# Kernel tuning notes

Measured on AMD Instinct MI355X. Metric: run time of the kernel, lower is better.

## Reference

```python
import jax, jax.numpy as jnp
import numpy as np

jax.config.update('jax_enable_x64', True)

RES = 0.1
HASH_SIZE = 2 ** 20
D = 120
HEADS = 8
HEAD_DIM = D // HEADS  # 15
MOD_T = 201
BMIN = np.array([-2.6, -8.1, 0.0], dtype=np.float32)
BMAX = np.array([4.6, 4.7, 3.1], dtype=np.float32)
PRIMES = np.array([73856093, 19349669, 83492791], dtype=np.int64)
M = 200000


def _build_buffer():
    axes = [np.arange(BMIN[i], BMAX[i], RES, dtype=np.float32) for i in range(3)]
    g = np.meshgrid(*axes, indexing='ij')
    coords = np.stack(g, axis=-1).reshape(-1, 3)
    n = coords.shape[0]
    grid = np.floor(coords / RES).astype(np.int64)
    h = np.remainder((grid * PRIMES).sum(-1), HASH_SIZE)
    buf = np.full(HASH_SIZE, n, dtype=np.int64)
    # loop assigns in increasing i and keeps the first => min index per hash slot
    np.minimum.at(buf, h, np.arange(n, dtype=np.int64))
    buf = np.where(buf == n, -1, buf)
    return buf, n


def setup_inputs() -> dict:
    key = jax.random.key(0)
    ks = jax.random.split(key, 9)
    buf, n_vox = _build_buffer()
    pts = jnp.asarray(BMIN) + jax.random.uniform(ks[0], (M, 3), dtype=jnp.float32) * jnp.asarray(BMAX - BMIN)
    times = jax.random.randint(ks[1], (M,), 0, 1000, dtype=jnp.int64)
    scale = float(1.0 / np.sqrt(D))
    return {
        'query_pts': pts,
        'query_times': times,
        'buffer_voxel_index': jnp.asarray(buf),
        'static_features': 0.01 * jax.random.normal(ks[2], (n_vox, D), dtype=jnp.float32),
        'dynamic_features': 0.01 * jax.random.normal(ks[3], (n_vox, D), dtype=jnp.float32),
        'time_embeddings': 0.01 * jax.random.normal(ks[4], (MOD_T, D), dtype=jnp.float32),
        'fusion_td_w': scale * jax.random.normal(ks[5], (4, D, D), dtype=jnp.float32),
        'fusion_td_b': jnp.zeros((4, D), dtype=jnp.float32),
        'fusion_sd_w': scale * jax.random.normal(ks[6], (4, D, D), dtype=jnp.float32),
        'fusion_sd_b': jnp.zeros((4, D), dtype=jnp.float32),
    }


def _fusion(a, b, W, B):
    # LocalSelfAttentionFusion: 2-token multi-head self-attention over [a; b],
    # returning the attended first token. W/B stack (q, k, v, out) projections.
    m = a.shape[0]
    tok = jnp.stack([a, b], axis=1)  # [M, 2, D]
    q = (tok @ W[0] + B[0]).reshape(m, 2, HEADS, HEAD_DIM)
    k = (tok @ W[1] + B[1]).reshape(m, 2, HEADS, HEAD_DIM)
    v = (tok @ W[2] + B[2]).reshape(m, 2, HEADS, HEAD_DIM)
    s = jnp.einsum('mqhd,mkhd->mhqk', q, k) * np.float32(1.0 / np.sqrt(HEAD_DIM))
    p = jax.nn.softmax(s, axis=-1)  # [M, H, 2, 2]
    o = jnp.einsum('mhqk,mkhd->mqhd', p, v).reshape(m, 2, D)
    return (o @ W[3] + B[3])[:, 0]  # fused token, [M, D]


def reference(query_pts, query_times, buffer_voxel_index, static_features, dynamic_features,
              time_embeddings, fusion_td_w, fusion_td_b, fusion_sd_w, fusion_sd_b):
    grid = jnp.floor(query_pts / RES).astype(jnp.int64)
    h = jnp.remainder((grid * jnp.asarray(PRIMES)).sum(-1), HASH_SIZE)
    v_idx = buffer_voxel_index[h]              # [M]
    valid = v_idx >= 0
    vi = jnp.where(valid, v_idx, 0)            # safe gather index
    ti = jnp.remainder(query_times, MOD_T)
    sf = static_features[vi]                   # [M, D]
    df = dynamic_features[vi]                  # [M, D]
    te = time_embeddings[ti]                   # [M, D]
    cond = _fusion(df, te, fusion_td_w, fusion_td_b)
    fused = _fusion(sf, cond, fusion_sd_w, fusion_sd_b)
    return jnp.where(valid[:, None], fused, jnp.float32(0))
```

## Files before the change

### kernel.cpp

```cpp
#include <hip/hip_runtime.h>
#include <math.h>

#define DD   120
#define KPAD 128
#define KP   136
#define MT   64
#define NTHR 512
#define HASH_MASK 1048575LL
#define MODT 201

typedef short  short8  __attribute__((ext_vector_type(8)));
typedef float  floatx4 __attribute__((ext_vector_type(4)));

__device__ __forceinline__ unsigned short f2b(float f) {
    __bf16 h = (__bf16)f;
    return __builtin_bit_cast(unsigned short, h);
}
__device__ __forceinline__ float b2f(unsigned short u) {
    unsigned int x = ((unsigned int)u) << 16;
    return __builtin_bit_cast(float, x);
}

__global__ __launch_bounds__(256)
void prep_weights(const float* __restrict__ td_w, const float* __restrict__ sd_w,
                  unsigned short* __restrict__ wt)
{
    int idx = blockIdx.x * 256 + threadIdx.x;
    int mat = idx >> 14;
    int n   = (idx >> 7) & 127;
    int k   = idx & 127;
    const float* src = (mat < 4) ? (td_w + mat * DD * DD) : (sd_w + (mat - 4) * DD * DD);
    float v = (n < DD && k < DD) ? src[k * DD + n] : 0.f;
    wt[idx] = f2b(v);
}

__global__ __launch_bounds__(128)
void prep_te(const float* __restrict__ temb, const float* __restrict__ td_w,
             const float* __restrict__ td_b,
             unsigned short* __restrict__ k1t, unsigned short* __restrict__ v1t)
{
    int t = blockIdx.x;
    int n = threadIdx.x;
    float a1 = 0.f, a2 = 0.f;
    if (n < DD) {
        a1 = td_b[DD + n];
        a2 = td_b[2 * DD + n];
        const float* te = temb + t * DD;
        const float* w1 = td_w + 1 * DD * DD;
        const float* w2 = td_w + 2 * DD * DD;
        for (int k = 0; k < DD; k++) {
            float x = te[k];
            a1 = fmaf(x, w1[k * DD + n], a1);
            a2 = fmaf(x, w2[k * DD + n], a2);
        }
    }
    k1t[t * KPAD + n] = f2b(a1);
    v1t[t * KPAD + n] = f2b(a2);
}

__device__ __forceinline__ void gemm_tile(const unsigned short* IN,
                                          const unsigned short* __restrict__ WT,
                                          const float* __restrict__ bias,
                                          unsigned short* OUT,
                                          int lm, int lq, int n0)
{
    const int n = n0 + lm;
    short8 bfr[4];
#pragma unroll
    for (int ks = 0; ks < 4; ks++)
        bfr[ks] = *(const short8*)(WT + n * KPAD + ks * 32 + lq * 8);
    float bv = (n < DD) ? bias[n] : 0.f;
#pragma unroll
    for (int mt = 0; mt < 4; mt++) {
        floatx4 acc = {0.f, 0.f, 0.f, 0.f};
#pragma unroll
        for (int ks = 0; ks < 4; ks++) {
            short8 a = *(const short8*)(IN + (mt * 16 + lm) * KP + ks * 32 + lq * 8);
            acc = __builtin_amdgcn_mfma_f32_16x16x32_bf16(a, bfr[ks], acc, 0, 0, 0);
        }
#pragma unroll
        for (int r = 0; r < 4; r++)
            OUT[(mt * 16 + lq * 4 + r) * KP + n] = f2b(acc[r] + bv);
    }
}

__device__ __forceinline__ void gemm_out(const unsigned short* IN,
                                         const unsigned short* __restrict__ WT,
                                         const float* __restrict__ bias,
                                         float* __restrict__ out,
                                         const int* s_valid, int pbase, int Mpts,
                                         int lm, int lq, int n0)
{
    const int n = n0 + lm;
    short8 bfr[4];
#pragma unroll
    for (int ks = 0; ks < 4; ks++)
        bfr[ks] = *(const short8*)(WT + n * KPAD + ks * 32 + lq * 8);
    float bv = (n < DD) ? bias[n] : 0.f;
#pragma unroll
    for (int mt = 0; mt < 4; mt++) {
        floatx4 acc = {0.f, 0.f, 0.f, 0.f};
#pragma unroll
        for (int ks = 0; ks < 4; ks++) {
            short8 a = *(const short8*)(IN + (mt * 16 + lm) * KP + ks * 32 + lq * 8);
            acc = __builtin_amdgcn_mfma_f32_16x16x32_bf16(a, bfr[ks], acc, 0, 0, 0);
        }
        if (n < DD) {
#pragma unroll
            for (int r = 0; r < 4; r++) {
                int row = mt * 16 + lq * 4 + r;
                int gp = pbase + row;
                if (gp < Mpts)
                    out[(size_t)gp * DD + n] = s_valid[row] ? (acc[r] + bv) : 0.f;
            }
        }
    }
}

__device__ __forceinline__ void attn(const unsigned short* Q, const unsigned short* K0,
                                     const unsigned short* K1, const unsigned short* V0,
                                     const unsigned short* V1, unsigned short* DEST,
                                     int tid)
{
    int p = tid >> 3, h = tid & 7;
    int base = p * KP + h * 15;
    float s0 = 0.f, s1 = 0.f;
#pragma unroll
    for (int j = 0; j < 15; j++) {
        float q = b2f(Q[base + j]);
        s0 = fmaf(q, b2f(K0[base + j]), s0);
        s1 = fmaf(q, b2f(K1[base + j]), s1);
    }
    const float scale = 0.2581988897471611f;
    s0 *= scale; s1 *= scale;
    float mx = fmaxf(s0, s1);
    float e0 = expf(s0 - mx), e1 = expf(s1 - mx);
    float p0 = e0 / (e0 + e1);
#pragma unroll
    for (int j = 0; j < 15; j++) {
        int nn = p * KP + h * 15 + j;
        float v = p0 * b2f(V0[nn]) + (1.f - p0) * b2f(V1[nn]);
        DEST[nn] = f2b(v);
    }
    if (h == 0) *(uint4*)(DEST + p * KP + 120) = make_uint4(0u, 0u, 0u, 0u);
}

__global__ __launch_bounds__(NTHR, 1)
void voxel_mfma_kernel(const float* __restrict__ pts,
                       const int* __restrict__ times,
                       const int* __restrict__ vox_buf,
                       const float* __restrict__ stat_f,
                       const float* __restrict__ dyn_f,
                       const float* __restrict__ td_b,
                       const float* __restrict__ sd_b,
                       const unsigned short* __restrict__ wt,
                       const unsigned short* __restrict__ k1t,
                       const unsigned short* __restrict__ v1t,
                       float* __restrict__ out,
                       int Mpts)
{
    __shared__ __align__(16) unsigned short A [MT * KP];
    __shared__ __align__(16) unsigned short P1[MT * KP];
    __shared__ __align__(16) unsigned short P2[MT * KP];
    __shared__ __align__(16) unsigned short P3[MT * KP];
    __shared__ __align__(16) unsigned short P4[MT * KP];
    __shared__ __align__(16) unsigned short P5[MT * KP];
    __shared__ int s_vi[MT];
    __shared__ int s_valid[MT];
    __shared__ int s_ti[MT];

    const int tid = threadIdx.x;
    const int lane = tid & 63;
    const int lm = lane & 15;
    const int lq = lane >> 4;
    const int n0 = (tid >> 6) * 16;
    const int pbase = blockIdx.x * MT;

    if (tid < MT) {
        int p = pbase + tid;
        int vi = 0, valid = 0, ti = 0;
        if (p < Mpts) {
            float x = pts[3 * p + 0];
            float y = pts[3 * p + 1];
            float z = pts[3 * p + 2];
            long long gx = (long long)floorf(x / 0.1f);
            long long gy = (long long)floorf(y / 0.1f);
            long long gz = (long long)floorf(z / 0.1f);
            long long hh = (gx * 73856093LL + gy * 19349669LL + gz * 83492791LL) & HASH_MASK;
            int v = vox_buf[(int)hh];
            valid = (v >= 0) ? 1 : 0;
            vi = (v >= 0) ? v : 0;
            ti = times[p] % MODT;
        }
        s_vi[tid] = vi; s_valid[tid] = valid; s_ti[tid] = ti;
    }
    if (tid < MT * 2) {
        int p = tid >> 1, hh = tid & 1;
        *(uint2*)(A + p * KP + 120 + hh * 4) = make_uint2(0u, 0u);
    }
    __syncthreads();

    for (int i = tid; i < MT * 30; i += NTHR) {
        int p = i / 30, f = i % 30;
        float4 v = *(const float4*)(dyn_f + (size_t)s_vi[p] * DD + f * 4);
        unsigned int lo = (unsigned int)f2b(v.x) | ((unsigned int)f2b(v.y) << 16);
        unsigned int hi = (unsigned int)f2b(v.z) | ((unsigned int)f2b(v.w) << 16);
        *(uint2*)(A + p * KP + f * 4) = make_uint2(lo, hi);
    }
    for (int i = tid; i < MT * 16; i += NTHR) {
        int p = i >> 4, f = i & 15;
        *(uint4*)(P4 + p * KP + f * 8) = *(const uint4*)(k1t + s_ti[p] * KPAD + f * 8);
        *(uint4*)(P5 + p * KP + f * 8) = *(const uint4*)(v1t + s_ti[p] * KPAD + f * 8);
    }
    __syncthreads();

    gemm_tile(A, wt + 0 * 16384, td_b + 0,   P1, lm, lq, n0);
    gemm_tile(A, wt + 1 * 16384, td_b + 120, P2, lm, lq, n0);
    gemm_tile(A, wt + 2 * 16384, td_b + 240, P3, lm, lq, n0);
    __syncthreads();

    attn(P1, P2, P4, P3, P5, A, tid);
    __syncthreads();

    gemm_tile(A, wt + 3 * 16384, td_b + 360, P1, lm, lq, n0);
    __syncthreads();

    for (int i = tid; i < MT * 30; i += NTHR) {
        int p = i / 30, f = i % 30;
        float4 v = *(const float4*)(stat_f + (size_t)s_vi[p] * DD + f * 4);
        unsigned int lo = (unsigned int)f2b(v.x) | ((unsigned int)f2b(v.y) << 16);
        unsigned int hi = (unsigned int)f2b(v.z) | ((unsigned int)f2b(v.w) << 16);
        *(uint2*)(A + p * KP + f * 4) = make_uint2(lo, hi);
    }
    __syncthreads();

    gemm_tile(A,  wt + 4 * 16384, sd_b + 0,   P2, lm, lq, n0);
    gemm_tile(A,  wt + 5 * 16384, sd_b + 120, P3, lm, lq, n0);
    gemm_tile(A,  wt + 6 * 16384, sd_b + 240, P4, lm, lq, n0);
    gemm_tile(P1, wt + 5 * 16384, sd_b + 120, P5, lm, lq, n0);
    __syncthreads();
    gemm_tile(P1, wt + 6 * 16384, sd_b + 240, A,  lm, lq, n0);
    __syncthreads();

    attn(P2, P3, P5, P4, A, P1, tid);
    __syncthreads();

    gemm_out(P1, wt + 7 * 16384, sd_b + 360, out, s_valid, pbase, Mpts, lm, lq, n0);
}

extern "C" void kernel_launch(void* const* d_in, const int* in_sizes, int n_in,
                              void* d_out, int out_size, void* d_ws, size_t ws_size,
                              hipStream_t stream) {
    const float* pts   = (const float*)d_in[0];
    const int*   times = (const int*)d_in[1];
    const int*   vox   = (const int*)d_in[2];
    const float* statf = (const float*)d_in[3];
    const float* dynf  = (const float*)d_in[4];
    const float* temb  = (const float*)d_in[5];
    const float* td_w  = (const float*)d_in[6];
    const float* td_b  = (const float*)d_in[7];
    const float* sd_w  = (const float*)d_in[8];
    const float* sd_b  = (const float*)d_in[9];

    unsigned short* wt  = (unsigned short*)d_ws;
    unsigned short* k1t = wt + 8 * 128 * 128;
    unsigned short* v1t = k1t + 201 * 128;

    prep_weights<<<512, 256, 0, stream>>>(td_w, sd_w, wt);
    prep_te<<<201, 128, 0, stream>>>(temb, td_w, td_b, k1t, v1t);

    int Mpts = in_sizes[0] / 3;
    int blocks = (Mpts + MT - 1) / MT;
    voxel_mfma_kernel<<<blocks, NTHR, 0, stream>>>(
        pts, times, vox, statf, dynf, td_b, sd_b, wt, k1t, v1t,
        (float*)d_out, Mpts);
}
```

Baseline: 579.7 us.

## Pad heads to 16 lanes, cut LDS to four buffers, raise occupancy

Weights and biases are re-laid out so each attention head occupies a 16-wide aligned slot, which lets the attention steps use vectorised 16-element dot products and combines. K1/V1 time embeddings are read straight from global memory instead of being staged into LDS. The GEMM is restructured so each wave keeps A fragments in registers and swaps the MFMA operand order, which gives packed stores and float4 output writes. Shared memory drops from six tile buffers to four and launch bounds allow up to four blocks per CU, at the cost of more barriers and a reordered dataflow.

Result: slower. 766.3 us (+32.2%).

```diff
diff --git a/kernel.cpp b/kernel.cpp
--- a/kernel.cpp
+++ b/kernel.cpp
@@ -30,8 +30,33 @@
     int n   = (idx >> 7) & 127;
     int k   = idx & 127;
     const float* src = (mat < 4) ? (td_w + mat * DD * DD) : (sd_w + (mat - 4) * DD * DD);
-    float v = (n < DD && k < DD) ? src[k * DD + n] : 0.f;
+    float v = 0.f;
+    if (mat == 3 || mat == 7) {
+        int hk = k >> 4, jk = k & 15;
+        if (n < DD && jk < 15) v = src[(hk * 15 + jk) * DD + n];
+    } else {
+        int h = n >> 4, j = n & 15;
+        if (j < 15 && k < DD) v = src[k * DD + h * 15 + j];
+    }
     wt[idx] = f2b(v);
+}
+
+__global__ __launch_bounds__(128)
+void prep_bias(const float* __restrict__ td_b, const float* __restrict__ sd_b,
+               float* __restrict__ bp)
+{
+    int idx = blockIdx.x * 128 + threadIdx.x;
+    int mat = idx >> 7;
+    int n   = idx & 127;
+    const float* src = (mat < 4) ? (td_b + mat * DD) : (sd_b + (mat - 4) * DD);
+    float v = 0.f;
+    if (mat == 3 || mat == 7) {
+        if (n < DD) v = src[n];
+    } else {
+        int h = n >> 4, j = n & 15;
+        if (j < 15) v = src[h * 15 + j];
+    }
+    bp[idx] = v;
 }
 
 __global__ __launch_bounds__(128)
@@ -40,9 +65,11 @@
              unsigned short* __restrict__ k1t, unsigned short* __restrict__ v1t)
 {
     int t = blockIdx.x;
-    int n = threadIdx.x;
+    int np = threadIdx.x;
+    int h = np >> 4, j = np & 15;
     float a1 = 0.f, a2 = 0.f;
-    if (n < DD) {
+    if (j < 15) {
+        int n = h * 15 + j;
         a1 = td_b[DD + n];
         a2 = td_b[2 * DD + n];
         const float* te = temb + t * DD;
@@ -54,127 +81,138 @@
             a2 = fmaf(x, w2[k * DD + n], a2);
         }
     }
-    k1t[t * KPAD + n] = f2b(a1);
-    v1t[t * KPAD + n] = f2b(a2);
-}
-
-__device__ __forceinline__ void gemm_tile(const unsigned short* IN,
-                                          const unsigned short* __restrict__ WT,
-                                          const float* __restrict__ bias,
-                                          unsigned short* OUT,
-                                          int lm, int lq, int n0)
-{
-    const int n = n0 + lm;
-    short8 bfr[4];
-#pragma unroll
-    for (int ks = 0; ks < 4; ks++)
-        bfr[ks] = *(const short8*)(WT + n * KPAD + ks * 32 + lq * 8);
-    float bv = (n < DD) ? bias[n] : 0.f;
-#pragma unroll
-    for (int mt = 0; mt < 4; mt++) {
+    k1t[t * KPAD + np] = f2b(a1);
+    v1t[t * KPAD + np] = f2b(a2);
+}
+
+__device__ __forceinline__ void gemm4(const unsigned short* IN,
+                                      const unsigned short* __restrict__ W,
+                                      const float* __restrict__ BP,
+                                      unsigned short* OUT,
+                                      int mg, int nh, int lm, int lq)
+{
+    short8 af[4];
+    const unsigned short* abase = IN + (mg * 16 + lm) * KP + lq * 8;
+#pragma unroll
+    for (int ks = 0; ks < 4; ks++) af[ks] = *(const short8*)(abase + ks * 32);
+#pragma unroll
+    for (int nt = 0; nt < 4; nt++) {
+        const unsigned short* wbase = W + (nh * 64 + nt * 16 + lm) * KPAD + lq * 8;
         floatx4 acc = {0.f, 0.f, 0.f, 0.f};
 #pragma unroll
         for (int ks = 0; ks < 4; ks++) {
-            short8 a = *(const short8*)(IN + (mt * 16 + lm) * KP + ks * 32 + lq * 8);
-            acc = __builtin_amdgcn_mfma_f32_16x16x32_bf16(a, bfr[ks], acc, 0, 0, 0);
-        }
-#pragma unroll
-        for (int r = 0; r < 4; r++)
-            OUT[(mt * 16 + lq * 4 + r) * KP + n] = f2b(acc[r] + bv);
-    }
-}
-
-__device__ __forceinline__ void gemm_out(const unsigned short* IN,
-                                         const unsigned short* __restrict__ WT,
-                                         const float* __restrict__ bias,
-                                         float* __restrict__ out,
-                                         const int* s_valid, int pbase, int Mpts,
-                                         int lm, int lq, int n0)
-{
-    const int n = n0 + lm;
-    short8 bfr[4];
-#pragma unroll
-    for (int ks = 0; ks < 4; ks++)
-        bfr[ks] = *(const short8*)(WT + n * KPAD + ks * 32 + lq * 8);
-    float bv = (n < DD) ? bias[n] : 0.f;
-#pragma unroll
-    for (int mt = 0; mt < 4; mt++) {
+            short8 wf = *(const short8*)(wbase + ks * 32);
+            acc = __builtin_amdgcn_mfma_f32_16x16x32_bf16(wf, af[ks], acc, 0, 0, 0);
+        }
+        int nc = nh * 64 + nt * 16 + lq * 4;
+        float4 b4 = *(const float4*)(BP + nc);
+        unsigned int lo = (unsigned)f2b(acc[0] + b4.x) | ((unsigned)f2b(acc[1] + b4.y) << 16);
+        unsigned int hi = (unsigned)f2b(acc[2] + b4.z) | ((unsigned)f2b(acc[3] + b4.w) << 16);
+        *(uint2*)(OUT + (mg * 16 + lm) * KP + nc) = make_uint2(lo, hi);
+    }
+}
+
+__device__ __forceinline__ void gemm_final(const unsigned short* IN,
+                                           const unsigned short* __restrict__ W,
+                                           const float* __restrict__ BP,
+                                           float* __restrict__ out,
+                                           const int* s_valid, int pbase, int Mpts,
+                                           int mg, int nh, int lm, int lq)
+{
+    short8 af[4];
+    const unsigned short* abase = IN + (mg * 16 + lm) * KP + lq * 8;
+#pragma unroll
+    for (int ks = 0; ks < 4; ks++) af[ks] = *(const short8*)(abase + ks * 32);
+    int row = mg * 16 + lm;
+    int gp = pbase + row;
+    int vmask = s_valid[row];
+#pragma unroll
+    for (int nt = 0; nt < 4; nt++) {
+        const unsigned short* wbase = W + (nh * 64 + nt * 16 + lm) * KPAD + lq * 8;
         floatx4 acc = {0.f, 0.f, 0.f, 0.f};
 #pragma unroll
         for (int ks = 0; ks < 4; ks++) {
-            short8 a = *(const short8*)(IN + (mt * 16 + lm) * KP + ks * 32 + lq * 8);
-            acc = __builtin_amdgcn_mfma_f32_16x16x32_bf16(a, bfr[ks], acc, 0, 0, 0);
-        }
-        if (n < DD) {
-#pragma unroll
-            for (int r = 0; r < 4; r++) {
-                int row = mt * 16 + lq * 4 + r;
-                int gp = pbase + row;
-                if (gp < Mpts)
-                    out[(size_t)gp * DD + n] = s_valid[row] ? (acc[r] + bv) : 0.f;
-            }
-        }
-    }
-}
-
-__device__ __forceinline__ void attn(const unsigned short* Q, const unsigned short* K0,
-                                     const unsigned short* K1, const unsigned short* V0,
-                                     const unsigned short* V1, unsigned short* DEST,
-                                     int tid)
-{
-    int p = tid >> 3, h = tid & 7;
-    int base = p * KP + h * 15;
-    float s0 = 0.f, s1 = 0.f;
-#pragma unroll
-    for (int j = 0; j < 15; j++) {
-        float q = b2f(Q[base + j]);
-        s0 = fmaf(q, b2f(K0[base + j]), s0);
-        s1 = fmaf(q, b2f(K1[base + j]), s1);
-    }
-    const float scale = 0.2581988897471611f;
-    s0 *= scale; s1 *= scale;
-    float mx = fmaxf(s0, s1);
-    float e0 = expf(s0 - mx), e1 = expf(s1 - mx);
-    float p0 = e0 / (e0 + e1);
-#pragma unroll
-    for (int j = 0; j < 15; j++) {
-        int nn = p * KP + h * 15 + j;
-        float v = p0 * b2f(V0[nn]) + (1.f - p0) * b2f(V1[nn]);
-        DEST[nn] = f2b(v);
-    }
-    if (h == 0) *(uint4*)(DEST + p * KP + 120) = make_uint4(0u, 0u, 0u, 0u);
-}
-
-__global__ __launch_bounds__(NTHR, 1)
+            short8 wf = *(const short8*)(wbase + ks * 32);
+            acc = __builtin_amdgcn_mfma_f32_16x16x32_bf16(wf, af[ks], acc, 0, 0, 0);
+        }
+        int nc = nh * 64 + nt * 16 + lq * 4;
+        if (nc < DD && gp < Mpts) {
+            float4 b4 = *(const float4*)(BP + nc);
+            float4 o;
+            o.x = vmask ? (acc[0] + b4.x) : 0.f;
+            o.y = vmask ? (acc[1] + b4.y) : 0.f;
+            o.z = vmask ? (acc[2] + b4.z) : 0.f;
+            o.w = vmask ? (acc[3] + b4.w) : 0.f;
+            *(float4*)(out + (size_t)gp * DD + nc) = o;
+        }
+    }
+}
+
+__device__ __forceinline__ float dot16u(const unsigned short* A_, const unsigned short* B_)
+{
+    float s = 0.f;
+#pragma unroll
+    for (int half = 0; half < 2; half++) {
+        short8 a = *(const short8*)(A_ + half * 8);
+        short8 b = *(const short8*)(B_ + half * 8);
+#pragma unroll
+        for (int i = 0; i < 8; i++)
+            s = fmaf(b2f((unsigned short)a[i]), b2f((unsigned short)b[i]), s);
+    }
+    return s;
+}
+
+__device__ __forceinline__ void comb16(unsigned short* dst, const unsigned short* v0,
+                                       const unsigned short* v1, float p0)
+{
+    float q0 = 1.f - p0;
+#pragma unroll
+    for (int half = 0; half < 2; half++) {
+        short8 a = *(const short8*)(v0 + half * 8);
+        short8 b = *(const short8*)(v1 + half * 8);
+        unsigned int w[4];
+#pragma unroll
+        for (int q = 0; q < 4; q++) {
+            float lo = p0 * b2f((unsigned short)a[2 * q])     + q0 * b2f((unsigned short)b[2 * q]);
+            float hi = p0 * b2f((unsigned short)a[2 * q + 1]) + q0 * b2f((unsigned short)b[2 * q + 1]);
+            w[q] = (unsigned)f2b(lo) | ((unsigned)f2b(hi) << 16);
+        }
+        *(uint4*)(dst + half * 8) = make_uint4(w[0], w[1], w[2], w[3]);
+    }
+}
+
+__global__ __launch_bounds__(NTHR, 4)
 void voxel_mfma_kernel(const float* __restrict__ pts,
                        const int* __restrict__ times,
                        const int* __restrict__ vox_buf,
                        const float* __restrict__ stat_f,
                        const float* __restrict__ dyn_f,
-                       const float* __restrict__ td_b,
-                       const float* __restrict__ sd_b,
                        const unsigned short* __restrict__ wt,
+                       const float* __restrict__ bp,
                        const unsigned short* __restrict__ k1t,
                        const unsigned short* __restrict__ v1t,
                        float* __restrict__ out,
                        int Mpts)
 {
-    __shared__ __align__(16) unsigned short A [MT * KP];
-    __shared__ __align__(16) unsigned short P1[MT * KP];
-    __shared__ __align__(16) unsigned short P2[MT * KP];
-    __shared__ __align__(16) unsigned short P3[MT * KP];
-    __shared__ __align__(16) unsigned short P4[MT * KP];
-    __shared__ __align__(16) unsigned short P5[MT * KP];
+    __shared__ __align__(16) unsigned short LA[MT * KP];
+    __shared__ __align__(16) unsigned short LB[MT * KP];
+    __shared__ __align__(16) unsigned short LC[MT * KP];
+    __shared__ __align__(16) unsigned short LD[MT * KP];
+    __shared__ float sc_p0[MT][8];
+    __shared__ float sc_s0[MT][8];
     __shared__ int s_vi[MT];
     __shared__ int s_valid[MT];
     __shared__ int s_ti[MT];
 
-    const int tid = threadIdx.x;
+    const int tid  = threadIdx.x;
     const int lane = tid & 63;
-    const int lm = lane & 15;
-    const int lq = lane >> 4;
-    const int n0 = (tid >> 6) * 16;
+    const int lm   = lane & 15;
+    const int lq   = lane >> 4;
+    const int wid  = tid >> 6;
+    const int mg   = wid >> 1;
+    const int nh   = wid & 1;
     const int pbase = blockIdx.x * MT;
+    const float scale = 0.2581988897471611f;
 
     if (tid < MT) {
         int p = pbase + tid;
@@ -194,58 +232,91 @@
         }
         s_vi[tid] = vi; s_valid[tid] = valid; s_ti[tid] = ti;
     }
-    if (tid < MT * 2) {
-        int p = tid >> 1, hh = tid & 1;
-        *(uint2*)(A + p * KP + 120 + hh * 4) = make_uint2(0u, 0u);
-    }
-    __syncthreads();
-
-    for (int i = tid; i < MT * 30; i += NTHR) {
-        int p = i / 30, f = i % 30;
-        float4 v = *(const float4*)(dyn_f + (size_t)s_vi[p] * DD + f * 4);
-        unsigned int lo = (unsigned int)f2b(v.x) | ((unsigned int)f2b(v.y) << 16);
-        unsigned int hi = (unsigned int)f2b(v.z) | ((unsigned int)f2b(v.w) << 16);
-        *(uint2*)(A + p * KP + f * 4) = make_uint2(lo, hi);
-    }
-    for (int i = tid; i < MT * 16; i += NTHR) {
-        int p = i >> 4, f = i & 15;
-        *(uint4*)(P4 + p * KP + f * 8) = *(const uint4*)(k1t + s_ti[p] * KPAD + f * 8);
-        *(uint4*)(P5 + p * KP + f * 8) = *(const uint4*)(v1t + s_ti[p] * KPAD + f * 8);
-    }
-    __syncthreads();
-
-    gemm_tile(A, wt + 0 * 16384, td_b + 0,   P1, lm, lq, n0);
-    gemm_tile(A, wt + 1 * 16384, td_b + 120, P2, lm, lq, n0);
-    gemm_tile(A, wt + 2 * 16384, td_b + 240, P3, lm, lq, n0);
-    __syncthreads();
-
-    attn(P1, P2, P4, P3, P5, A, tid);
-    __syncthreads();
-
-    gemm_tile(A, wt + 3 * 16384, td_b + 360, P1, lm, lq, n0);
-    __syncthreads();
-
-    for (int i = tid; i < MT * 30; i += NTHR) {
-        int p = i / 30, f = i % 30;
-        float4 v = *(const float4*)(stat_f + (size_t)s_vi[p] * DD + f * 4);
-        unsigned int lo = (unsigned int)f2b(v.x) | ((unsigned int)f2b(v.y) << 16);
-        unsigned int hi = (unsigned int)f2b(v.z) | ((unsigned int)f2b(v.w) << 16);
-        *(uint2*)(A + p * KP + f * 4) = make_uint2(lo, hi);
-    }
-    __syncthreads();
-
-    gemm_tile(A,  wt + 4 * 16384, sd_b + 0,   P2, lm, lq, n0);
-    gemm_tile(A,  wt + 5 * 16384, sd_b + 120, P3, lm, lq, n0);
-    gemm_tile(A,  wt + 6 * 16384, sd_b + 240, P4, lm, lq, n0);
-    gemm_tile(P1, wt + 5 * 16384, sd_b + 120, P5, lm, lq, n0);
-    __syncthreads();
-    gemm_tile(P1, wt + 6 * 16384, sd_b + 240, A,  lm, lq, n0);
-    __syncthreads();
-
-    attn(P2, P3, P5, P4, A, P1, tid);
-    __syncthreads();
-
-    gemm_out(P1, wt + 7 * 16384, sd_b + 360, out, s_valid, pbase, Mpts, lm, lq, n0);
+    __syncthreads();
+
+    for (int i = tid; i < MT * 32; i += NTHR) {
+        int p = i >> 5, f = i & 31;
+        if (f < 30) {
+            float4 v = *(const float4*)(dyn_f + (size_t)s_vi[p] * DD + f * 4);
+            unsigned int lo = (unsigned)f2b(v.x) | ((unsigned)f2b(v.y) << 16);
+            unsigned int hi = (unsigned)f2b(v.z) | ((unsigned)f2b(v.w) << 16);
+            *(uint2*)(LA + p * KP + f * 4) = make_uint2(lo, hi);
+        } else if (f == 30) {
+            *(uint4*)(LA + p * KP + 120) = make_uint4(0u, 0u, 0u, 0u);
+        }
+    }
+    __syncthreads();
+
+    gemm4(LA, wt + 0 * 16384, bp + 0 * 128, LB, mg, nh, lm, lq);
+    gemm4(LA, wt + 1 * 16384, bp + 1 * 128, LC, mg, nh, lm, lq);
+    gemm4(LA, wt + 2 * 16384, bp + 2 * 128, LD, mg, nh, lm, lq);
+    __syncthreads();
+
+    {
+        int p = tid >> 3, h = tid & 7;
+        const unsigned short* qp  = LB + p * KP + h * 16;
+        const unsigned short* k0p = LC + p * KP + h * 16;
+        const unsigned short* k1p = k1t + s_ti[p] * KPAD + h * 16;
+        float s0 = dot16u(qp, k0p) * scale;
+        float s1 = dot16u(qp, k1p) * scale;
+        sc_p0[p][h] = 1.f / (1.f + expf(s1 - s0));
+    }
+    for (int i = tid; i < MT * 32; i += NTHR) {
+        int p = i >> 5, f = i & 31;
+        if (f < 30) {
+            float4 v = *(const float4*)(stat_f + (size_t)s_vi[p] * DD + f * 4);
+            unsigned int lo = (unsigned)f2b(v.x) | ((unsigned)f2b(v.y) << 16);
+            unsigned int hi = (unsigned)f2b(v.z) | ((unsigned)f2b(v.w) << 16);
+            *(uint2*)(LA + p * KP + f * 4) = make_uint2(lo, hi);
+        } else if (f == 30) {
+            *(uint4*)(LA + p * KP + 120) = make_uint4(0u, 0u, 0u, 0u);
+        }
+    }
+    __syncthreads();
+
+    {
+        int p = tid >> 3, sg = tid & 7;
+        comb16(LC + p * KP + sg * 16, LD + p * KP + sg * 16,
+               v1t + s_ti[p] * KPAD + sg * 16, sc_p0[p][sg]);
+    }
+    __syncthreads();
+
+    gemm4(LC, wt + 3 * 16384, bp + 3 * 128, LB, mg, nh, lm, lq);
+    __syncthreads();
+
+    gemm4(LA, wt + 4 * 16384, bp + 4 * 128, LD, mg, nh, lm, lq);
+    gemm4(LA, wt + 5 * 16384, bp + 5 * 128, LC, mg, nh, lm, lq);
+    __syncthreads();
+
+    {
+        int p = tid >> 3, h = tid & 7;
+        sc_s0[p][h] = dot16u(LD + p * KP + h * 16, LC + p * KP + h * 16) * scale;
+    }
+    __syncthreads();
+
+    gemm4(LB, wt + 5 * 16384, bp + 5 * 128, LC, mg, nh, lm, lq);
+    __syncthreads();
+
+    {
+        int p = tid >> 3, h = tid & 7;
+        float s1 = dot16u(LD + p * KP + h * 16, LC + p * KP + h * 16) * scale;
+        sc_p0[p][h] = 1.f / (1.f + expf(s1 - sc_s0[p][h]));
+    }
+    __syncthreads();
+
+    gemm4(LA, wt + 6 * 16384, bp + 6 * 128, LD, mg, nh, lm, lq);
+    gemm4(LB, wt + 6 * 16384, bp + 6 * 128, LC, mg, nh, lm, lq);
+    __syncthreads();
+
+    {
+        int p = tid >> 3, sg = tid & 7;
+        comb16(LA + p * KP + sg * 16, LD + p * KP + sg * 16,
+               LC + p * KP + sg * 16, sc_p0[p][sg]);
+    }
+    __syncthreads();
+
+    gemm_final(LA, wt + 7 * 16384, bp + 7 * 128, out, s_valid, pbase, Mpts,
+               mg, nh, lm, lq);
 }
 
 extern "C" void kernel_launch(void* const* d_in, const int* in_sizes, int n_in,
@@ -263,15 +334,17 @@
     const float* sd_b  = (const float*)d_in[9];
 
     unsigned short* wt  = (unsigned short*)d_ws;
-    unsigned short* k1t = wt + 8 * 128 * 128;
+    float*          bpf = (float*)(wt + 8 * 128 * 128);
+    unsigned short* k1t = (unsigned short*)(bpf + 8 * 128);
     unsigned short* v1t = k1t + 201 * 128;
 
     prep_weights<<<512, 256, 0, stream>>>(td_w, sd_w, wt);
+    prep_bias<<<8, 128, 0, stream>>>(td_b, sd_b, bpf);
     prep_te<<<201, 128, 0, stream>>>(temb, td_w, td_b, k1t, v1t);
 
     int Mpts = in_sizes[0] / 3;
     int blocks = (Mpts + MT - 1) / MT;
     voxel_mfma_kernel<<<blocks, NTHR, 0, stream>>>(
-        pts, times, vox, statf, dynf, td_b, sd_b, wt, k1t, v1t,
+        pts, times, vox, statf, dynf, wt, bpf, k1t, v1t,
         (float*)d_out, Mpts);
 }
```
